# Kernel tuning notes

Hardware: AMD Instinct MI355X
Metric: run time of the kernel (lower is better)

The kernel has to match this reference:

```python
import jax, jax.numpy as jnp
import numpy as np

N_NODES = 50000
N_EDGES = 400000
N_GRAPHS = 512
NF = 64      # node_features
EF = 32      # edge_features (RBF bins)
AIF = 92     # atom_input_features
FC = 128     # fc_features
L = 3        # conv layers
EPS = 1e-5   # BatchNorm eps


def _bn(x, gamma, beta):
    # BatchNorm1d, training-mode statistics over the batch (edge/node) dim
    m = x.mean(0)
    v = x.var(0)  # biased variance, matches torch normalization
    return (x - m) * jax.lax.rsqrt(v + EPS) * gamma + beta


def _rbf(d):
    # RBFExpansion(vmin=0, vmax=8, bins=EF): gamma = 1/mean(diff(centers))
    centers = jnp.linspace(0.0, 8.0, EF)
    gamma = 1.0 / (centers[1] - centers[0])
    return jnp.exp(-gamma * (d[:, None] - centers) ** 2)  # [E, EF]


def setup_inputs() -> dict:
    key = jax.random.key(0)
    ks = jax.random.split(key, 12)
    s = 0.05
    IN = 2 * NF + EF
    return {
        "atom_features": jax.random.normal(ks[0], (N_NODES, AIF), dtype=jnp.float32),
        "bondlength": jax.random.uniform(ks[1], (N_EDGES,), dtype=jnp.float32) * 8.0,
        "src": jax.random.randint(ks[2], (N_EDGES,), 0, N_NODES),
        "dst": jax.random.randint(ks[3], (N_EDGES,), 0, N_NODES),
        "graph_ids": jnp.sort(jax.random.randint(ks[4], (N_NODES,), 0, N_GRAPHS)),
        "W_emb": jax.random.normal(ks[5], (AIF, NF), dtype=jnp.float32) * s,
        "b_emb": jnp.zeros((NF,), jnp.float32),
        "Wi": jax.random.normal(ks[6], (L, IN, NF), dtype=jnp.float32) * s,
        "bi": jnp.zeros((L, NF), jnp.float32),
        "gi": jnp.ones((L, NF), jnp.float32),
        "bti": jnp.zeros((L, NF), jnp.float32),
        "Wu": jax.random.normal(ks[7], (L, IN, NF), dtype=jnp.float32) * s,
        "bu": jnp.zeros((L, NF), jnp.float32),
        "gu": jnp.ones((L, NF), jnp.float32),
        "btu": jnp.zeros((L, NF), jnp.float32),
        "g_bn": jnp.ones((L, NF), jnp.float32),
        "b_bn": jnp.zeros((L, NF), jnp.float32),
        "W_fc": jax.random.normal(ks[8], (NF, FC), dtype=jnp.float32) * s,
        "b_fc": jnp.zeros((FC,), jnp.float32),
        "W_out": jax.random.normal(ks[9], (FC, 1), dtype=jnp.float32) * s,
        "b_out": jnp.zeros((1,), jnp.float32),
    }


def reference(atom_features, bondlength, src, dst, graph_ids,
              W_emb, b_emb, Wi, bi, gi, bti, Wu, bu, gu, btu,
              g_bn, b_bn, W_fc, b_fc, W_out, b_out):
    e = _rbf(bondlength)                       # [E, EF]
    h = atom_features @ W_emb + b_emb          # [N, NF]
    for l in range(L):
        # gather + concat: [E, 2*NF + EF]
        z = jnp.concatenate([h[src], h[dst], e], axis=1)
        gate = jax.nn.sigmoid(_bn(z @ Wi[l] + bi[l], gi[l], bti[l]))
        upd = jax.nn.softplus(_bn(z @ Wu[l] + bu[l], gu[l], btu[l]))
        msg = gate * upd                       # [E, NF]
        agg = jax.ops.segment_sum(msg, dst, num_segments=N_NODES)
        h = jax.nn.softplus(h + _bn(agg, g_bn[l], b_bn[l]))
    # AvgPooling over nodes per graph
    counts = jax.ops.segment_sum(jnp.ones((N_NODES, 1), h.dtype), graph_ids,
                                 num_segments=N_GRAPHS)
    pooled = jax.ops.segment_sum(h, graph_ids, num_segments=N_GRAPHS)
    pooled = pooled / jnp.maximum(counts, 1.0)  # [G, NF]
    f = jax.nn.softplus(pooled)
    f = jax.nn.softplus(f @ W_fc + b_fc)
    f = jax.nn.softplus(f)
    out = f @ W_out + b_out                    # [G, 1]
    return jnp.squeeze(out)                    # [G]
```

## Files before the change

kernel.cpp:

```cpp
#include <hip/hip_runtime.h>
#include <math.h>

#define N_NODES 50000
#define N_EDGES 400000
#define N_GRAPHS 512
#define TBL 2048
#define EPSBN 1e-5f

__device__ __forceinline__ float softplusf(float x) {
  return fmaxf(x, 0.0f) + log1pf(expf(-fabsf(x)));
}
__device__ __forceinline__ float sigmoidf(float x) {
  return 1.0f / (1.0f + expf(-x));
}
__device__ __forceinline__ void fma4(float4& acc, float s, const float4& w) {
  acc.x = fmaf(s, w.x, acc.x);
  acc.y = fmaf(s, w.y, acc.y);
  acc.z = fmaf(s, w.z, acc.z);
  acc.w = fmaf(s, w.w, acc.w);
}

__global__ void k_emb(const float* __restrict__ atom,
                      const float* __restrict__ Wemb,
                      const float* __restrict__ bemb,
                      float* __restrict__ h) {
  __shared__ float sW[92 * 64];
  __shared__ float sA[32 * 92];
  const int tid = threadIdx.x;
  for (int i = tid; i < 92 * 64; i += 256) sW[i] = Wemb[i];

  const int t0 = blockIdx.x * 32;
  const int nt = min(32, N_NODES - t0);
  {
    const float* srcp = atom + (size_t)t0 * 92;
    const int tot = nt * 92;
    for (int i = tid; i < tot; i += 256) sA[i] = srcp[i];
  }
  __syncthreads();

  const int col = tid & 63;
  const int ng = tid >> 6;
  const float bb = bemb[col];
  float acc[8];
#pragma unroll
  for (int i = 0; i < 8; ++i) acc[i] = bb;

  for (int kc = 0; kc < 92; kc += 4) {
    const float w0 = sW[(kc + 0) * 64 + col];
    const float w1 = sW[(kc + 1) * 64 + col];
    const float w2 = sW[(kc + 2) * 64 + col];
    const float w3 = sW[(kc + 3) * 64 + col];
#pragma unroll
    for (int i = 0; i < 8; ++i) {
      const float4 a = *(const float4*)&sA[(ng * 8 + i) * 92 + kc];
      acc[i] = fmaf(a.x, w0, acc[i]);
      acc[i] = fmaf(a.y, w1, acc[i]);
      acc[i] = fmaf(a.z, w2, acc[i]);
      acc[i] = fmaf(a.w, w3, acc[i]);
    }
  }
#pragma unroll
  for (int i = 0; i < 8; ++i) {
    const int n = t0 + ng * 8 + i;
    if (n < N_NODES) h[(size_t)n * 64 + col] = acc[i];
  }
}

__global__ void k_pq(const float* __restrict__ h,
                     const float* __restrict__ Wi_l,
                     const float* __restrict__ Wu_l,
                     float* __restrict__ PA,
                     float* __restrict__ PB) {
  __shared__ float sWA[64 * 128];
  __shared__ float sWB[64 * 128];
  __shared__ float sH[32 * 64];
  const int tid = threadIdx.x;

  for (int i = tid; i < 64 * 64; i += 256) {
    const int k = i >> 6, c = i & 63;
    sWA[k * 128 + c]      = Wi_l[k * 64 + c];
    sWA[k * 128 + 64 + c] = Wu_l[k * 64 + c];
    sWB[k * 128 + c]      = Wi_l[(64 + k) * 64 + c];
    sWB[k * 128 + 64 + c] = Wu_l[(64 + k) * 64 + c];
  }
  const int t0 = blockIdx.x * 32;
  const int nt = min(32, N_NODES - t0);
  {
    const float4* srcp = (const float4*)(h + (size_t)t0 * 64);
    const int tot4 = nt * 16;
    float4* dstp = (float4*)sH;
    for (int i = tid; i < tot4; i += 256) dstp[i] = srcp[i];
  }
  __syncthreads();

  const int wave = tid >> 6, lane = tid & 63;
  const float* wcol = (lane < 32) ? (sWA + 4 * lane) : (sWB + 4 * (lane - 32));
  const int jj = (lane < 32) ? 4 * lane : 4 * (lane - 32);
  float* OUTb = (lane < 32) ? PA : PB;

  float4 acc[8];
#pragma unroll
  for (int i = 0; i < 8; ++i) acc[i] = make_float4(0.f, 0.f, 0.f, 0.f);

  for (int kc = 0; kc < 64; kc += 4) {
    const float4 w0 = *(const float4*)(wcol + (kc + 0) * 128);
    const float4 w1 = *(const float4*)(wcol + (kc + 1) * 128);
    const float4 w2 = *(const float4*)(wcol + (kc + 2) * 128);
    const float4 w3 = *(const float4*)(wcol + (kc + 3) * 128);
#pragma unroll
    for (int i = 0; i < 8; ++i) {
      const float4 a = *(const float4*)&sH[(wave * 8 + i) * 64 + kc];
      fma4(acc[i], a.x, w0);
      fma4(acc[i], a.y, w1);
      fma4(acc[i], a.z, w2);
      fma4(acc[i], a.w, w3);
    }
  }
#pragma unroll
  for (int i = 0; i < 8; ++i) {
    const int n = t0 + wave * 8 + i;
    if (n < N_NODES) *(float4*)&OUTb[(size_t)n * 128 + jj] = acc[i];
  }
}

__global__ void k_tbl(const float* __restrict__ Wi_l,
                      const float* __restrict__ Wu_l,
                      float* __restrict__ tbl) {
  const int wave = threadIdx.x >> 6, lane = threadIdx.x & 63;
  const int t = blockIdx.x * (blockDim.x >> 6) + wave;
  if (t >= TBL) return;
  const float d = 8.0f * (float)t / (float)(TBL - 1);
  float gi_ = 0.f, gu_ = 0.f;
#pragma unroll
  for (int k = 0; k < 32; ++k) {
    const float c = 8.0f * (float)k / 31.0f;
    const float dd = d - c;
    const float r = expf(-3.875f * dd * dd);
    gi_ = fmaf(r, Wi_l[(128 + k) * 64 + lane], gi_);
    gu_ = fmaf(r, Wu_l[(128 + k) * 64 + lane], gu_);
  }
  tbl[(size_t)t * 128 + lane] = gi_;
  tbl[(size_t)t * 128 + 64 + lane] = gu_;
}

__device__ __forceinline__ void edge_pre(int e, int lane,
                                         const int* __restrict__ src,
                                         const int* __restrict__ dst,
                                         const float* __restrict__ bond,
                                         const float* __restrict__ PA,
                                         const float* __restrict__ PB,
                                         const float* __restrict__ tbl,
                                         float& yg, float& yu, int& dnode) {
  const int s = src[e];
  const int d2 = dst[e];
  const float d = bond[e];
  float f = d * ((float)(TBL - 1) / 8.0f);
  f = fminf(fmaxf(f, 0.0f), (float)(TBL - 1));
  int i0 = (int)f;
  if (i0 > TBL - 2) i0 = TBL - 2;
  const float fr = f - (float)i0;
  const float* ta = tbl + (size_t)i0 * 128 + lane;
  const float rg = fmaf(fr, ta[128] - ta[0], ta[0]);
  const float ru = fmaf(fr, ta[192] - ta[64], ta[64]);
  const float* pa = PA + (size_t)s * 128 + lane;
  const float* pb = PB + (size_t)d2 * 128 + lane;
  yg = pa[0] + pb[0] + rg;
  yu = pa[64] + pb[64] + ru;
  dnode = d2;
}

__global__ void k_edge_stats(const int* __restrict__ src,
                             const int* __restrict__ dst,
                             const float* __restrict__ bond,
                             const float* __restrict__ PA,
                             const float* __restrict__ PB,
                             const float* __restrict__ tbl,
                             float* __restrict__ stats) {
  const int wave = threadIdx.x >> 6, lane = threadIdx.x & 63;
  const int wpb = blockDim.x >> 6;
  const int nw = wpb * gridDim.x;
  float sg = 0.f, qg = 0.f, su = 0.f, qu = 0.f;
  for (int e = blockIdx.x * wpb + wave; e < N_EDGES; e += nw) {
    float yg, yu; int dn;
    edge_pre(e, lane, src, dst, bond, PA, PB, tbl, yg, yu, dn);
    sg += yg; qg = fmaf(yg, yg, qg);
    su += yu; qu = fmaf(yu, yu, qu);
  }
  __shared__ float red[4][4][64];
  red[0][wave][lane] = sg;
  red[1][wave][lane] = qg;
  red[2][wave][lane] = su;
  red[3][wave][lane] = qu;
  __syncthreads();
  const float v = red[wave][0][lane] + red[wave][1][lane] +
                  red[wave][2][lane] + red[wave][3][lane];
  atomicAdd(&stats[wave * 64 + lane], v);
}

__global__ void k_fin_gu(const float* __restrict__ stats,
                         const float* __restrict__ gi_l, const float* __restrict__ bti_l,
                         const float* __restrict__ gu_l, const float* __restrict__ btu_l,
                         float* __restrict__ coefs) {
  const int j = threadIdx.x;
  const float invE = 1.0f / (float)N_EDGES;
  float m = stats[j] * invE;
  float v = stats[64 + j] * invE - m * m;
  float a = gi_l[j] * rsqrtf(v + EPSBN);
  coefs[j] = a;
  coefs[64 + j] = fmaf(-m, a, bti_l[j]);
  m = stats[128 + j] * invE;
  v = stats[192 + j] * invE - m * m;
  a = gu_l[j] * rsqrtf(v + EPSBN);
  coefs[128 + j] = a;
  coefs[192 + j] = fmaf(-m, a, btu_l[j]);
}

__global__ void k_edge_apply(const int* __restrict__ src,
                             const int* __restrict__ dst,
                             const float* __restrict__ bond,
                             const float* __restrict__ PA,
                             const float* __restrict__ PB,
                             const float* __restrict__ tbl,
                             const float* __restrict__ coefs,
                             float* __restrict__ agg) {
  const int wave = threadIdx.x >> 6, lane = threadIdx.x & 63;
  const int wpb = blockDim.x >> 6;
  const int nw = wpb * gridDim.x;
  const float ag = coefs[lane], bg = coefs[64 + lane];
  const float au = coefs[128 + lane], bu = coefs[192 + lane];
  for (int e = blockIdx.x * wpb + wave; e < N_EDGES; e += nw) {
    float yg, yu; int dn;
    edge_pre(e, lane, src, dst, bond, PA, PB, tbl, yg, yu, dn);
    const float gate = sigmoidf(fmaf(ag, yg, bg));
    const float upd = softplusf(fmaf(au, yu, bu));
    atomicAdd(&agg[(size_t)dn * 64 + lane], gate * upd);
  }
}

__global__ void k_agg_stats(const float* __restrict__ agg, float* __restrict__ stats) {
  const int wave = threadIdx.x >> 6, lane = threadIdx.x & 63;
  const int wpb = blockDim.x >> 6;
  const int nw = wpb * gridDim.x;
  float s = 0.f, q = 0.f;
  for (int n = blockIdx.x * wpb + wave; n < N_NODES; n += nw) {
    const float v = agg[(size_t)n * 64 + lane];
    s += v; q = fmaf(v, v, q);
  }
  __shared__ float red[2][4][64];
  red[0][wave][lane] = s;
  red[1][wave][lane] = q;
  __syncthreads();
  if (wave < 2) {
    const float v = red[wave][0][lane] + red[wave][1][lane] +
                    red[wave][2][lane] + red[wave][3][lane];
    atomicAdd(&stats[256 + wave * 64 + lane], v);
  }
}

__global__ void k_fin_agg(const float* __restrict__ stats,
                          const float* __restrict__ gbn_l, const float* __restrict__ bbn_l,
                          float* __restrict__ coefs) {
  const int j = threadIdx.x;
  const float invN = 1.0f / (float)N_NODES;
  const float m = stats[256 + j] * invN;
  const float v = stats[320 + j] * invN - m * m;
  const float a = gbn_l[j] * rsqrtf(v + EPSBN);
  coefs[256 + j] = a;
  coefs[320 + j] = fmaf(-m, a, bbn_l[j]);
}

__global__ void k_hupd(float* __restrict__ h, const float* __restrict__ agg,
                       const float* __restrict__ coefs) {
  const int stride = blockDim.x * gridDim.x;
  for (int i = blockIdx.x * blockDim.x + threadIdx.x; i < N_NODES * 64; i += stride) {
    const int j = i & 63;
    const float x = h[i] + fmaf(coefs[256 + j], agg[i], coefs[320 + j]);
    h[i] = softplusf(x);
  }
}

__global__ void k_pool(const float* __restrict__ h, const int* __restrict__ gid,
                       float* __restrict__ pooled, float* __restrict__ counts) {
  const int wave = threadIdx.x >> 6, lane = threadIdx.x & 63;
  const int wpb = blockDim.x >> 6;
  const int nw = wpb * gridDim.x;
  for (int n = blockIdx.x * wpb + wave; n < N_NODES; n += nw) {
    const int g = gid[n];
    atomicAdd(&pooled[(size_t)g * 64 + lane], h[(size_t)n * 64 + lane]);
    if (lane == 0) atomicAdd(&counts[g], 1.0f);
  }
}

__global__ void k_final(const float* __restrict__ pooled, const float* __restrict__ counts,
                        const float* __restrict__ Wfc, const float* __restrict__ bfc,
                        const float* __restrict__ Wout, const float* __restrict__ bout,
                        float* __restrict__ out) {
  __shared__ float f1[64];
  __shared__ float red[128];
  const int g = blockIdx.x, t = threadIdx.x;
  if (t < 64) {
    const float c = fmaxf(counts[g], 1.0f);
    f1[t] = softplusf(pooled[(size_t)g * 64 + t] / c);
  }
  __syncthreads();
  float acc = bfc[t];
#pragma unroll
  for (int k = 0; k < 64; ++k) acc = fmaf(f1[k], Wfc[k * 128 + t], acc);
  red[t] = softplusf(softplusf(acc)) * Wout[t];
  __syncthreads();
  for (int s2 = 64; s2 > 0; s2 >>= 1) {
    if (t < s2) red[t] += red[t + s2];
    __syncthreads();
  }
  if (t == 0) out[g] = red[0] + bout[0];
}

extern "C" void kernel_launch(void* const* d_in, const int* in_sizes, int n_in,
                              void* d_out, int out_size, void* d_ws, size_t ws_size,
                              hipStream_t stream) {
  const float* atom = (const float*)d_in[0];
  const float* bond = (const float*)d_in[1];
  const int* src = (const int*)d_in[2];
  const int* dst = (const int*)d_in[3];
  const int* gid = (const int*)d_in[4];
  const float* Wemb = (const float*)d_in[5];
  const float* bemb = (const float*)d_in[6];
  const float* Wi = (const float*)d_in[7];
  const float* gi = (const float*)d_in[9];
  const float* bti = (const float*)d_in[10];
  const float* Wu = (const float*)d_in[11];
  const float* gub = (const float*)d_in[13];
  const float* btu = (const float*)d_in[14];
  const float* gbn = (const float*)d_in[15];
  const float* bbn = (const float*)d_in[16];
  const float* Wfc = (const float*)d_in[17];
  const float* bfc = (const float*)d_in[18];
  const float* Wout = (const float*)d_in[19];
  const float* bout = (const float*)d_in[20];

  float* h = (float*)d_ws;
  float* PA = h + (size_t)N_NODES * 64;
  float* PB = PA + (size_t)N_NODES * 128;
  float* agg = PB + (size_t)N_NODES * 128;
  float* tbl = agg + (size_t)N_NODES * 64;
  float* stats = tbl + (size_t)TBL * 128;
  float* coefs = stats + 384;
  float* pooled = coefs + 384;
  float* counts = pooled + (size_t)N_GRAPHS * 64;

  const int ntiles = (N_NODES + 31) / 32;

  k_emb<<<ntiles, 256, 0, stream>>>(atom, Wemb, bemb, h);
  for (int l = 0; l < 3; ++l) {
    const float* Wi_l = Wi + (size_t)l * 160 * 64;
    const float* Wu_l = Wu + (size_t)l * 160 * 64;
    (void)hipMemsetAsync(stats, 0, 384 * sizeof(float), stream);
    (void)hipMemsetAsync(agg, 0, (size_t)N_NODES * 64 * sizeof(float), stream);
    k_pq<<<ntiles, 256, 0, stream>>>(h, Wi_l, Wu_l, PA, PB);
    k_tbl<<<TBL / 4, 256, 0, stream>>>(Wi_l, Wu_l, tbl);
    k_edge_stats<<<2048, 256, 0, stream>>>(src, dst, bond, PA, PB, tbl, stats);
    k_fin_gu<<<1, 64, 0, stream>>>(stats, gi + l * 64, bti + l * 64,
                                   gub + l * 64, btu + l * 64, coefs);
    k_edge_apply<<<2048, 256, 0, stream>>>(src, dst, bond, PA, PB, tbl, coefs, agg);
    k_agg_stats<<<512, 256, 0, stream>>>(agg, stats);
    k_fin_agg<<<1, 64, 0, stream>>>(stats, gbn + l * 64, bbn + l * 64, coefs);
    k_hupd<<<1024, 256, 0, stream>>>(h, agg, coefs);
  }
  (void)hipMemsetAsync(pooled, 0, (size_t)(N_GRAPHS * 64 + N_GRAPHS) * sizeof(float), stream);
  k_pool<<<512, 256, 0, stream>>>(h, gid, pooled, counts);
  k_final<<<N_GRAPHS, 128, 0, stream>>>(pooled, counts, Wfc, bfc, Wout, bout,
                                        (float*)d_out);
}
```

Before: 1.791 ms.

## Build dst-sorted CSR once and aggregate edges per node without atomics

```diff
diff --git a/kernel.cpp b/kernel.cpp
--- a/kernel.cpp
+++ b/kernel.cpp
@@ -18,6 +18,53 @@
   acc.y = fmaf(s, w.y, acc.y);
   acc.z = fmaf(s, w.z, acc.z);
   acc.w = fmaf(s, w.w, acc.w);
+}
+
+__global__ void k_hist(const int* __restrict__ dst, int* __restrict__ deg) {
+  const int e = blockIdx.x * blockDim.x + threadIdx.x;
+  if (e < N_EDGES) atomicAdd(&deg[dst[e]], 1);
+}
+
+__global__ void k_scan(const int* __restrict__ deg, int* __restrict__ rowptr,
+                       int* __restrict__ cursor) {
+  __shared__ int ssum[1024];
+  const int t = threadIdx.x;
+  const int strip = (N_NODES + 1023) / 1024;
+  const int a = t * strip;
+  const int b = min(N_NODES, a + strip);
+  int s = 0;
+  for (int i = a; i < b; ++i) s += deg[i];
+  ssum[t] = s;
+  __syncthreads();
+  if (t == 0) {
+    int run = 0;
+    for (int i = 0; i < 1024; ++i) {
+      const int x = ssum[i];
+      ssum[i] = run;
+      run += x;
+    }
+    rowptr[N_NODES] = run;
+  }
+  __syncthreads();
+  int run = ssum[t];
+  for (int i = a; i < b; ++i) {
+    rowptr[i] = run;
+    cursor[i] = run;
+    run += deg[i];
+  }
+}
+
+__global__ void k_scatter(const int* __restrict__ src, const int* __restrict__ dst,
+                          const float* __restrict__ bond,
+                          int* __restrict__ cursor,
+                          int* __restrict__ csr_src, float* __restrict__ csr_f) {
+  const int e = blockIdx.x * blockDim.x + threadIdx.x;
+  if (e >= N_EDGES) return;
+  const int d2 = dst[e];
+  const int pos = atomicAdd(&cursor[d2], 1);
+  csr_src[pos] = src[e];
+  float f = bond[e] * ((float)(TBL - 1) / 8.0f);
+  csr_f[pos] = fminf(fmaxf(f, 0.0f), (float)(TBL - 1));
 }
 
 __global__ void k_emb(const float* __restrict__ atom,
@@ -28,7 +75,6 @@
   __shared__ float sA[32 * 92];
   const int tid = threadIdx.x;
   for (int i = tid; i < 92 * 64; i += 256) sW[i] = Wemb[i];
-
   const int t0 = blockIdx.x * 32;
   const int nt = min(32, N_NODES - t0);
   {
@@ -37,14 +83,12 @@
     for (int i = tid; i < tot; i += 256) sA[i] = srcp[i];
   }
   __syncthreads();
-
   const int col = tid & 63;
   const int ng = tid >> 6;
   const float bb = bemb[col];
   float acc[8];
 #pragma unroll
   for (int i = 0; i < 8; ++i) acc[i] = bb;
-
   for (int kc = 0; kc < 92; kc += 4) {
     const float w0 = sW[(kc + 0) * 64 + col];
     const float w1 = sW[(kc + 1) * 64 + col];
@@ -101,7 +145,6 @@
   float4 acc[8];
 #pragma unroll
   for (int i = 0; i < 8; ++i) acc[i] = make_float4(0.f, 0.f, 0.f, 0.f);
-
   for (int kc = 0; kc < 64; kc += 4) {
     const float4 w0 = *(const float4*)(wcol + (kc + 0) * 128);
     const float4 w1 = *(const float4*)(wcol + (kc + 1) * 128);
@@ -143,48 +186,37 @@
   tbl[(size_t)t * 128 + 64 + lane] = gu_;
 }
 
-__device__ __forceinline__ void edge_pre(int e, int lane,
-                                         const int* __restrict__ src,
-                                         const int* __restrict__ dst,
-                                         const float* __restrict__ bond,
-                                         const float* __restrict__ PA,
-                                         const float* __restrict__ PB,
-                                         const float* __restrict__ tbl,
-                                         float& yg, float& yu, int& dnode) {
-  const int s = src[e];
-  const int d2 = dst[e];
-  const float d = bond[e];
-  float f = d * ((float)(TBL - 1) / 8.0f);
-  f = fminf(fmaxf(f, 0.0f), (float)(TBL - 1));
-  int i0 = (int)f;
-  if (i0 > TBL - 2) i0 = TBL - 2;
-  const float fr = f - (float)i0;
-  const float* ta = tbl + (size_t)i0 * 128 + lane;
-  const float rg = fmaf(fr, ta[128] - ta[0], ta[0]);
-  const float ru = fmaf(fr, ta[192] - ta[64], ta[64]);
-  const float* pa = PA + (size_t)s * 128 + lane;
-  const float* pb = PB + (size_t)d2 * 128 + lane;
-  yg = pa[0] + pb[0] + rg;
-  yu = pa[64] + pb[64] + ru;
-  dnode = d2;
-}
-
-__global__ void k_edge_stats(const int* __restrict__ src,
-                             const int* __restrict__ dst,
-                             const float* __restrict__ bond,
+__global__ void k_edge_stats(const int* __restrict__ rowptr,
+                             const int* __restrict__ csr_src,
+                             const float* __restrict__ csr_f,
                              const float* __restrict__ PA,
                              const float* __restrict__ PB,
                              const float* __restrict__ tbl,
                              float* __restrict__ stats) {
   const int wave = threadIdx.x >> 6, lane = threadIdx.x & 63;
-  const int wpb = blockDim.x >> 6;
-  const int nw = wpb * gridDim.x;
+  const int wid = blockIdx.x * (blockDim.x >> 6) + wave;
+  const int nw = gridDim.x * (blockDim.x >> 6);
+  const float* PAj = PA + lane;
+  const float* tbj = tbl + lane;
   float sg = 0.f, qg = 0.f, su = 0.f, qu = 0.f;
-  for (int e = blockIdx.x * wpb + wave; e < N_EDGES; e += nw) {
-    float yg, yu; int dn;
-    edge_pre(e, lane, src, dst, bond, PA, PB, tbl, yg, yu, dn);
-    sg += yg; qg = fmaf(yg, yg, qg);
-    su += yu; qu = fmaf(yu, yu, qu);
+  for (int n = wid; n < N_NODES; n += nw) {
+    const int r0 = rowptr[n], r1 = rowptr[n + 1];
+    if (r0 == r1) continue;
+    const float pbg = PB[(size_t)n * 128 + lane];
+    const float pbu = PB[(size_t)n * 128 + 64 + lane];
+    for (int k = r0; k < r1; ++k) {
+      const int s = csr_src[k];
+      const float cf = csr_f[k];
+      const int i0 = min((int)cf, TBL - 2);
+      const float fr = cf - (float)i0;
+      const float* ta = tbj + (size_t)i0 * 128;
+      const float pag = PAj[(size_t)s * 128];
+      const float pau = PAj[(size_t)s * 128 + 64];
+      const float yg = pag + pbg + fmaf(fr, ta[128] - ta[0], ta[0]);
+      const float yu = pau + pbu + fmaf(fr, ta[192] - ta[64], ta[64]);
+      sg += yg; qg = fmaf(yg, yg, qg);
+      su += yu; qu = fmaf(yu, yu, qu);
+    }
   }
   __shared__ float red[4][4][64];
   red[0][wave][lane] = sg;
@@ -204,56 +236,64 @@
   const int j = threadIdx.x;
   const float invE = 1.0f / (float)N_EDGES;
   float m = stats[j] * invE;
-  float v = stats[64 + j] * invE - m * m;
+  float v = fmaxf(stats[64 + j] * invE - m * m, 0.0f);
   float a = gi_l[j] * rsqrtf(v + EPSBN);
   coefs[j] = a;
   coefs[64 + j] = fmaf(-m, a, bti_l[j]);
   m = stats[128 + j] * invE;
-  v = stats[192 + j] * invE - m * m;
+  v = fmaxf(stats[192 + j] * invE - m * m, 0.0f);
   a = gu_l[j] * rsqrtf(v + EPSBN);
   coefs[128 + j] = a;
   coefs[192 + j] = fmaf(-m, a, btu_l[j]);
 }
 
-__global__ void k_edge_apply(const int* __restrict__ src,
-                             const int* __restrict__ dst,
-                             const float* __restrict__ bond,
+__global__ void k_edge_apply(const int* __restrict__ rowptr,
+                             const int* __restrict__ csr_src,
+                             const float* __restrict__ csr_f,
                              const float* __restrict__ PA,
-                             const float* __restrict__ PB,
+                             float* PBm,
                              const float* __restrict__ tbl,
                              const float* __restrict__ coefs,
-                             float* __restrict__ agg) {
+                             float* __restrict__ stats) {
   const int wave = threadIdx.x >> 6, lane = threadIdx.x & 63;
-  const int wpb = blockDim.x >> 6;
-  const int nw = wpb * gridDim.x;
+  const int wid = blockIdx.x * (blockDim.x >> 6) + wave;
+  const int nw = gridDim.x * (blockDim.x >> 6);
   const float ag = coefs[lane], bg = coefs[64 + lane];
   const float au = coefs[128 + lane], bu = coefs[192 + lane];
-  for (int e = blockIdx.x * wpb + wave; e < N_EDGES; e += nw) {
-    float yg, yu; int dn;
-    edge_pre(e, lane, src, dst, bond, PA, PB, tbl, yg, yu, dn);
-    const float gate = sigmoidf(fmaf(ag, yg, bg));
-    const float upd = softplusf(fmaf(au, yu, bu));
-    atomicAdd(&agg[(size_t)dn * 64 + lane], gate * upd);
-  }
-}
-
-__global__ void k_agg_stats(const float* __restrict__ agg, float* __restrict__ stats) {
-  const int wave = threadIdx.x >> 6, lane = threadIdx.x & 63;
-  const int wpb = blockDim.x >> 6;
-  const int nw = wpb * gridDim.x;
-  float s = 0.f, q = 0.f;
-  for (int n = blockIdx.x * wpb + wave; n < N_NODES; n += nw) {
-    const float v = agg[(size_t)n * 64 + lane];
-    s += v; q = fmaf(v, v, q);
+  const float* PAj = PA + lane;
+  const float* tbj = tbl + lane;
+  float ssum = 0.f, sqsum = 0.f;
+  for (int n = wid; n < N_NODES; n += nw) {
+    const int r0 = rowptr[n], r1 = rowptr[n + 1];
+    float msum = 0.f;
+    if (r0 < r1) {
+      const float pbg = PBm[(size_t)n * 128 + lane];
+      const float pbu = PBm[(size_t)n * 128 + 64 + lane];
+      for (int k = r0; k < r1; ++k) {
+        const int s = csr_src[k];
+        const float cf = csr_f[k];
+        const int i0 = min((int)cf, TBL - 2);
+        const float fr = cf - (float)i0;
+        const float* ta = tbj + (size_t)i0 * 128;
+        const float pag = PAj[(size_t)s * 128];
+        const float pau = PAj[(size_t)s * 128 + 64];
+        const float yg = pag + pbg + fmaf(fr, ta[128] - ta[0], ta[0]);
+        const float yu = pau + pbu + fmaf(fr, ta[192] - ta[64], ta[64]);
+        msum += sigmoidf(fmaf(ag, yg, bg)) * softplusf(fmaf(au, yu, bu));
+      }
+    }
+    PBm[(size_t)n * 128 + lane] = msum;
+    ssum += msum;
+    sqsum = fmaf(msum, msum, sqsum);
   }
   __shared__ float red[2][4][64];
-  red[0][wave][lane] = s;
-  red[1][wave][lane] = q;
+  red[0][wave][lane] = ssum;
+  red[1][wave][lane] = sqsum;
   __syncthreads();
   if (wave < 2) {
-    const float v = red[wave][0][lane] + red[wave][1][lane] +
-                    red[wave][2][lane] + red[wave][3][lane];
-    atomicAdd(&stats[256 + wave * 64 + lane], v);
+    const float vv = red[wave][0][lane] + red[wave][1][lane] +
+                     red[wave][2][lane] + red[wave][3][lane];
+    atomicAdd(&stats[256 + wave * 64 + lane], vv);
   }
 }
 
@@ -263,18 +303,19 @@
   const int j = threadIdx.x;
   const float invN = 1.0f / (float)N_NODES;
   const float m = stats[256 + j] * invN;
-  const float v = stats[320 + j] * invN - m * m;
+  const float v = fmaxf(stats[320 + j] * invN - m * m, 0.0f);
   const float a = gbn_l[j] * rsqrtf(v + EPSBN);
   coefs[256 + j] = a;
   coefs[320 + j] = fmaf(-m, a, bbn_l[j]);
 }
 
-__global__ void k_hupd(float* __restrict__ h, const float* __restrict__ agg,
+__global__ void k_hupd(float* __restrict__ h, const float* __restrict__ PBm,
                        const float* __restrict__ coefs) {
   const int stride = blockDim.x * gridDim.x;
   for (int i = blockIdx.x * blockDim.x + threadIdx.x; i < N_NODES * 64; i += stride) {
     const int j = i & 63;
-    const float x = h[i] + fmaf(coefs[256 + j], agg[i], coefs[320 + j]);
+    const int n = i >> 6;
+    const float x = h[i] + fmaf(coefs[256 + j], PBm[(size_t)n * 128 + j], coefs[320 + j]);
     h[i] = softplusf(x);
   }
 }
@@ -341,32 +382,42 @@
   float* h = (float*)d_ws;
   float* PA = h + (size_t)N_NODES * 64;
   float* PB = PA + (size_t)N_NODES * 128;
-  float* agg = PB + (size_t)N_NODES * 128;
-  float* tbl = agg + (size_t)N_NODES * 64;
+  float* tbl = PB + (size_t)N_NODES * 128;
   float* stats = tbl + (size_t)TBL * 128;
   float* coefs = stats + 384;
-  float* pooled = coefs + 384;
+  int* deg = (int*)(coefs + 384);
+  float* pooled = (float*)(deg + N_NODES);
   float* counts = pooled + (size_t)N_GRAPHS * 64;
+  int* rowptr = (int*)(counts + N_GRAPHS);
+  int* cursor = rowptr + N_NODES + 1;
+  int* csr_src = cursor + N_NODES;
+  float* csr_f = (float*)(csr_src + N_EDGES);
 
   const int ntiles = (N_NODES + 31) / 32;
+  const int egrid = (N_EDGES + 255) / 256;
+
+  (void)hipMemsetAsync(deg, 0,
+                       (size_t)(N_NODES + N_GRAPHS * 64 + N_GRAPHS) * 4, stream);
+  k_hist<<<egrid, 256, 0, stream>>>(dst, deg);
+  k_scan<<<1, 1024, 0, stream>>>(deg, rowptr, cursor);
+  k_scatter<<<egrid, 256, 0, stream>>>(src, dst, bond, cursor, csr_src, csr_f);
 
   k_emb<<<ntiles, 256, 0, stream>>>(atom, Wemb, bemb, h);
   for (int l = 0; l < 3; ++l) {
     const float* Wi_l = Wi + (size_t)l * 160 * 64;
     const float* Wu_l = Wu + (size_t)l * 160 * 64;
     (void)hipMemsetAsync(stats, 0, 384 * sizeof(float), stream);
-    (void)hipMemsetAsync(agg, 0, (size_t)N_NODES * 64 * sizeof(float), stream);
     k_pq<<<ntiles, 256, 0, stream>>>(h, Wi_l, Wu_l, PA, PB);
     k_tbl<<<TBL / 4, 256, 0, stream>>>(Wi_l, Wu_l, tbl);
-    k_edge_stats<<<2048, 256, 0, stream>>>(src, dst, bond, PA, PB, tbl, stats);
+    k_edge_stats<<<1024, 256, 0, stream>>>(rowptr, csr_src, csr_f,
+                                           PA, PB, tbl, stats);
     k_fin_gu<<<1, 64, 0, stream>>>(stats, gi + l * 64, bti + l * 64,
                                    gub + l * 64, btu + l * 64, coefs);
-    k_edge_apply<<<2048, 256, 0, stream>>>(src, dst, bond, PA, PB, tbl, coefs, agg);
-    k_agg_stats<<<512, 256, 0, stream>>>(agg, stats);
+    k_edge_apply<<<1024, 256, 0, stream>>>(rowptr, csr_src, csr_f,
+                                           PA, PB, tbl, coefs, stats);
     k_fin_agg<<<1, 64, 0, stream>>>(stats, gbn + l * 64, bbn + l * 64, coefs);
-    k_hupd<<<1024, 256, 0, stream>>>(h, agg, coefs);
-  }
-  (void)hipMemsetAsync(pooled, 0, (size_t)(N_GRAPHS * 64 + N_GRAPHS) * sizeof(float), stream);
+    k_hupd<<<1024, 256, 0, stream>>>(h, PB, coefs);
+  }
   k_pool<<<512, 256, 0, stream>>>(h, gid, pooled, counts);
   k_final<<<N_GRAPHS, 128, 0, stream>>>(pooled, counts, Wfc, bfc, Wout, bout,
                                         (float*)d_out);
```

Result: slower. 1.915 ms (+6.9%).
